# Kernel tuning notes

Hardware: AMD Instinct MI355X
Metric: run time of the kernel (lower is better)

## Reference

```python
import jax, jax.numpy as jnp
import numpy as np

B, N, C_IN = 8, 2048, 64
NUM_TERMS, NUM_CHANNELS = 3, 64
LN_EPS = 1e-5


def setup_inputs() -> dict:
    key = jax.random.key(0)
    k1, k2, k3 = jax.random.split(key, 3)
    A = jax.random.normal(k1, (B, N, N), dtype=jnp.float32) / jnp.sqrt(N).astype(jnp.float32)
    X = jax.random.normal(k2, (B, N, C_IN), dtype=jnp.float32)
    # xavier_uniform on h of shape [num_terms+1, num_channels, num_nodes]
    fan_in, fan_out = NUM_CHANNELS, N
    bound = float(np.sqrt(6.0 / (fan_in + fan_out)))
    h = jax.random.uniform(k3, (NUM_TERMS + 1, NUM_CHANNELS, N), dtype=jnp.float32,
                           minval=-bound, maxval=bound)
    gamma = jnp.ones((NUM_CHANNELS,), dtype=jnp.float32)
    beta = jnp.zeros((NUM_CHANNELS,), dtype=jnp.float32)
    return {"A": A, "X": X, "h": h, "gamma": gamma, "beta": beta}


def reference(A, X, h, gamma, beta):
    # Original loops compute: Y[b,n,c] = sum_i h[i,c,n] * (A^i @ sum_ch X[...,ch])[b,n]
    num_terms = h.shape[0] - 1
    Xs = X.sum(axis=-1)  # [B, N] -- inner channel loop collapses to a sum

    def step(p, _):
        p_next = jnp.einsum('bmn,bn->bm', A, p)  # A^i @ Xs
        return p_next, p_next

    _, Ps = jax.lax.scan(step, Xs, None, length=num_terms)  # [T, B, N]
    P = jnp.concatenate([Xs[None], Ps], axis=0)  # [T+1, B, N], P[0] = I @ Xs

    Y = jnp.einsum('icn,ibn->bnc', h, P)  # [B, N, C]

    mean = Y.mean(axis=-1, keepdims=True)
    var = Y.var(axis=-1, keepdims=True)
    Yn = (Y - mean) * jax.lax.rsqrt(var + LN_EPS) * gamma + beta
    return jnp.tanh(Yn)
```

## Files before the change

kernel.cpp:

```cpp
#include <hip/hip_runtime.h>
#include <hip/hip_bf16.h>
#include <hip/hip_fp16.h>
#include <math.h>

#define BB 8
#define NN 2048
#define C_IN 64
#define NCH 64
#define NTERMS 3
#define LN_EPS 1e-5f

__global__ void xsum_kernel(const float* __restrict__ X, float* __restrict__ Xs) {
    int row  = (blockIdx.x * blockDim.x + threadIdx.x) >> 6;
    int lane = threadIdx.x & 63;
    float v = X[(size_t)row * C_IN + lane];
    #pragma unroll
    for (int off = 32; off > 0; off >>= 1)
        v += __shfl_down(v, off, 64);
    if (lane == 0) Xs[row] = v;
}

__global__ __launch_bounds__(256, 4) void matvec_cvt_kernel(
        const float* __restrict__ A,
        const float* __restrict__ pin,
        float* __restrict__ pout,
        __half* __restrict__ A16) {
    const int b    = blockIdx.y;
    const int wave = threadIdx.x >> 6;
    const int lane = threadIdx.x & 63;
    const int m    = blockIdx.x * 4 + wave;

    const float4* pin4 = (const float4*)(pin + (size_t)b * NN);
    const float4* Ar   = (const float4*)(A + (size_t)b * NN * NN + (size_t)m * NN);

    float4 x[8], pr[8];
    #pragma unroll
    for (int j = 0; j < 8; ++j) x[j]  = Ar[j * 64 + lane];
    #pragma unroll
    for (int j = 0; j < 8; ++j) pr[j] = pin4[j * 64 + lane];

    float acc = 0.f;
    #pragma unroll
    for (int j = 0; j < 8; ++j)
        acc += x[j].x * pr[j].x + x[j].y * pr[j].y + x[j].z * pr[j].z + x[j].w * pr[j].w;

    float2* A16r = (float2*)(A16 + (size_t)b * NN * NN + (size_t)m * NN);
    #pragma unroll
    for (int j = 0; j < 8; ++j) {
        union { float2 f2; __half2 h2[2]; } u;
        u.h2[0] = __floats2half2_rn(x[j].x, x[j].y);
        u.h2[1] = __floats2half2_rn(x[j].z, x[j].w);
        A16r[j * 64 + lane] = u.f2;
    }

    #pragma unroll
    for (int off = 32; off > 0; off >>= 1)
        acc += __shfl_down(acc, off, 64);
    if (lane == 0) pout[(size_t)b * NN + m] = acc;
}

__global__ __launch_bounds__(256, 4) void matvec16_kernel(
        const __half* __restrict__ A16,
        const float* __restrict__ pin,
        float* __restrict__ pout) {
    const int b    = blockIdx.y;
    const int wave = threadIdx.x >> 6;
    const int lane = threadIdx.x & 63;
    const int m    = blockIdx.x * 4 + wave;

    const float4* pin4 = (const float4*)(pin + (size_t)b * NN);
    const float4* Ar   = (const float4*)(A16 + (size_t)b * NN * NN + (size_t)m * NN);

    float4 xr[4], pa[4], pb[4];
    #pragma unroll
    for (int j = 0; j < 4; ++j) xr[j] = Ar[j * 64 + lane];
    #pragma unroll
    for (int j = 0; j < 4; ++j) {
        pa[j] = pin4[2 * (j * 64 + lane)];
        pb[j] = pin4[2 * (j * 64 + lane) + 1];
    }

    float acc = 0.f;
    #pragma unroll
    for (int j = 0; j < 4; ++j) {
        const __half2* hx = (const __half2*)&xr[j];
        float2 f0 = __half22float2(hx[0]);
        float2 f1 = __half22float2(hx[1]);
        float2 f2 = __half22float2(hx[2]);
        float2 f3 = __half22float2(hx[3]);
        acc += f0.x * pa[j].x + f0.y * pa[j].y + f1.x * pa[j].z + f1.y * pa[j].w
             + f2.x * pb[j].x + f2.y * pb[j].y + f3.x * pb[j].z + f3.y * pb[j].w;
    }

    #pragma unroll
    for (int off = 32; off > 0; off >>= 1)
        acc += __shfl_down(acc, off, 64);
    if (lane == 0) pout[(size_t)b * NN + m] = acc;
}

__global__ __launch_bounds__(512) void combine_kernel(
        const float* __restrict__ h,
        const float* __restrict__ P,
        const float* __restrict__ gamma,
        const float* __restrict__ beta,
        float* __restrict__ out) {
    const int n    = blockIdx.x;
    const int b    = threadIdx.x >> 6;
    const int lane = threadIdx.x & 63;
    const int idx  = b * NN + n;

    const float p0 = P[0 * BB * NN + idx];
    const float p1 = P[1 * BB * NN + idx];
    const float p2 = P[2 * BB * NN + idx];
    const float p3 = P[3 * BB * NN + idx];

    float y = h[(size_t)(0 * NCH + lane) * NN + n] * p0
            + h[(size_t)(1 * NCH + lane) * NN + n] * p1
            + h[(size_t)(2 * NCH + lane) * NN + n] * p2
            + h[(size_t)(3 * NCH + lane) * NN + n] * p3;

    float s = y;
    #pragma unroll
    for (int off = 32; off > 0; off >>= 1)
        s += __shfl_xor(s, off, 64);
    const float mean = s * (1.f / NCH);

    float d = y - mean;
    float vs = d * d;
    #pragma unroll
    for (int off = 32; off > 0; off >>= 1)
        vs += __shfl_xor(vs, off, 64);
    const float rstd = rsqrtf(vs * (1.f / NCH) + LN_EPS);

    out[(size_t)idx * NCH + lane] = tanhf(d * rstd * gamma[lane] + beta[lane]);
}

extern "C" void kernel_launch(void* const* d_in, const int* in_sizes, int n_in,
                              void* d_out, int out_size, void* d_ws, size_t ws_size,
                              hipStream_t stream) {
    const float* A     = (const float*)d_in[0];
    const float* X     = (const float*)d_in[1];
    const float* h     = (const float*)d_in[2];
    const float* gamma = (const float*)d_in[3];
    const float* beta  = (const float*)d_in[4];
    float* out = (float*)d_out;

    float*  P   = (float*)d_ws;
    __half* A16 = (__half*)((char*)d_ws + (1u << 20));

    xsum_kernel<<<(BB * NN) / 4, 256, 0, stream>>>(X, P);

    dim3 mv_grid(NN / 4, BB);
    matvec_cvt_kernel<<<mv_grid, 256, 0, stream>>>(A, P, P + BB * NN, A16);

    for (int i = 2; i <= NTERMS; ++i) {
        matvec16_kernel<<<mv_grid, 256, 0, stream>>>(
            A16, P + (size_t)(i - 1) * BB * NN, P + (size_t)i * BB * NN);
    }

    combine_kernel<<<NN, 512, 0, stream>>>(h, P, gamma, beta, out);
}
```

Measured before the change: 249.3 us.

## Fuse all stages into one cooperative persistent kernel with grid syncs

Replaces the five separate launches (channel sum, fp32 matvec with fp16 conversion, two fp16 matvecs, layernorm combine) with one cooperative kernel of 256 blocks of 1024 threads that uses grid.sync between power iterations. Each block stages the input vector in shared memory and keeps its own rows' results in shared memory, so the final combine and layernorm need no extra pass over P. This removes launch gaps and repeated global vector reads, but adds grid-wide barrier cost. Only 256 blocks of 16 waves are used, so each wave processes four rows in sequence, which may cut the memory parallelism available for streaming A.

```diff
diff --git a/kernel.cpp b/kernel.cpp
--- a/kernel.cpp
+++ b/kernel.cpp
@@ -1,138 +1,181 @@
 #include <hip/hip_runtime.h>
-#include <hip/hip_bf16.h>
 #include <hip/hip_fp16.h>
+#include <hip/hip_cooperative_groups.h>
 #include <math.h>
+
+namespace cg = cooperative_groups;
 
 #define BB 8
 #define NN 2048
 #define C_IN 64
 #define NCH 64
-#define NTERMS 3
 #define LN_EPS 1e-5f
 
-__global__ void xsum_kernel(const float* __restrict__ X, float* __restrict__ Xs) {
-    int row  = (blockIdx.x * blockDim.x + threadIdx.x) >> 6;
-    int lane = threadIdx.x & 63;
-    float v = X[(size_t)row * C_IN + lane];
-    #pragma unroll
-    for (int off = 32; off > 0; off >>= 1)
-        v += __shfl_down(v, off, 64);
-    if (lane == 0) Xs[row] = v;
-}
+__global__ __launch_bounds__(1024, 4) void fused_kernel(
+        const float* __restrict__ A,
+        const float* __restrict__ X,
+        const float* __restrict__ h,
+        const float* __restrict__ gamma,
+        const float* __restrict__ beta,
+        float* __restrict__ out,
+        float* __restrict__ P,
+        __half* __restrict__ A16) {
+    cg::grid_group grid = cg::this_grid();
 
-__global__ __launch_bounds__(256, 4) void matvec_cvt_kernel(
-        const float* __restrict__ A,
-        const float* __restrict__ pin,
-        float* __restrict__ pout,
-        __half* __restrict__ A16) {
-    const int b    = blockIdx.y;
+    const int blk  = blockIdx.x;
     const int wave = threadIdx.x >> 6;
     const int lane = threadIdx.x & 63;
-    const int m    = blockIdx.x * 4 + wave;
+    const int b    = blk >> 5;
+    const int n0   = (blk & 31) * 64;
 
-    const float4* pin4 = (const float4*)(pin + (size_t)b * NN);
-    const float4* Ar   = (const float4*)(A + (size_t)b * NN * NN + (size_t)m * NN);
+    __shared__ float p[NN];
+    __shared__ float pl[4][64];
 
-    float4 x[8], pr[8];
     #pragma unroll
-    for (int j = 0; j < 8; ++j) x[j]  = Ar[j * 64 + lane];
-    #pragma unroll
-    for (int j = 0; j < 8; ++j) pr[j] = pin4[j * 64 + lane];
+    for (int i = 0; i < 4; ++i) {
+        const int n = n0 + wave * 4 + i;
+        float v = X[((size_t)b * NN + n) * C_IN + lane];
+        #pragma unroll
+        for (int off = 32; off > 0; off >>= 1)
+            v += __shfl_down(v, off, 64);
+        if (lane == 0) { P[b * NN + n] = v; pl[0][wave * 4 + i] = v; }
+    }
+    grid.sync();
 
-    float acc = 0.f;
-    #pragma unroll
-    for (int j = 0; j < 8; ++j)
-        acc += x[j].x * pr[j].x + x[j].y * pr[j].y + x[j].z * pr[j].z + x[j].w * pr[j].w;
+    {
+        float4* p4 = (float4*)p;
+        const float4* src = (const float4*)(P + b * NN);
+        if (threadIdx.x < NN / 4) p4[threadIdx.x] = src[threadIdx.x];
+        __syncthreads();
 
-    float2* A16r = (float2*)(A16 + (size_t)b * NN * NN + (size_t)m * NN);
-    #pragma unroll
-    for (int j = 0; j < 8; ++j) {
-        union { float2 f2; __half2 h2[2]; } u;
-        u.h2[0] = __floats2half2_rn(x[j].x, x[j].y);
-        u.h2[1] = __floats2half2_rn(x[j].z, x[j].w);
-        A16r[j * 64 + lane] = u.f2;
+        #pragma unroll
+        for (int i = 0; i < 4; ++i) {
+            const int m = n0 + wave * 4 + i;
+            const float4* Ar = (const float4*)(A + (size_t)b * NN * NN + (size_t)m * NN);
+            float4 x[8];
+            #pragma unroll
+            for (int j = 0; j < 8; ++j) x[j] = Ar[j * 64 + lane];
+
+            float acc = 0.f;
+            #pragma unroll
+            for (int j = 0; j < 8; ++j) {
+                float4 pv = p4[j * 64 + lane];
+                acc += x[j].x * pv.x + x[j].y * pv.y + x[j].z * pv.z + x[j].w * pv.w;
+            }
+
+            float2* A16r = (float2*)(A16 + (size_t)b * NN * NN + (size_t)m * NN);
+            #pragma unroll
+            for (int j = 0; j < 8; ++j) {
+                union { float2 f2; __half2 h2[2]; } u;
+                u.h2[0] = __floats2half2_rn(x[j].x, x[j].y);
+                u.h2[1] = __floats2half2_rn(x[j].z, x[j].w);
+                A16r[j * 64 + lane] = u.f2;
+            }
+
+            #pragma unroll
+            for (int off = 32; off > 0; off >>= 1)
+                acc += __shfl_down(acc, off, 64);
+            if (lane == 0) { P[(BB + b) * NN + m] = acc; pl[1][wave * 4 + i] = acc; }
+        }
+    }
+    grid.sync();
+
+    {
+        float4* p4 = (float4*)p;
+        const float4* src = (const float4*)(P + (BB + b) * NN);
+        if (threadIdx.x < NN / 4) p4[threadIdx.x] = src[threadIdx.x];
+        __syncthreads();
+
+        #pragma unroll
+        for (int i = 0; i < 4; ++i) {
+            const int m = n0 + wave * 4 + i;
+            const float4* Ar = (const float4*)(A16 + (size_t)b * NN * NN + (size_t)m * NN);
+            float4 xr[4];
+            #pragma unroll
+            for (int j = 0; j < 4; ++j) xr[j] = Ar[j * 64 + lane];
+
+            float acc = 0.f;
+            #pragma unroll
+            for (int j = 0; j < 4; ++j) {
+                float4 pa = p4[2 * (j * 64 + lane)];
+                float4 pb = p4[2 * (j * 64 + lane) + 1];
+                const __half2* hx = (const __half2*)&xr[j];
+                float2 f0 = __half22float2(hx[0]);
+                float2 f1 = __half22float2(hx[1]);
+                float2 f2 = __half22float2(hx[2]);
+                float2 f3 = __half22float2(hx[3]);
+                acc += f0.x * pa.x + f0.y * pa.y + f1.x * pa.z + f1.y * pa.w
+                     + f2.x * pb.x + f2.y * pb.y + f3.x * pb.z + f3.y * pb.w;
+            }
+
+            #pragma unroll
+            for (int off = 32; off > 0; off >>= 1)
+                acc += __shfl_down(acc, off, 64);
+            if (lane == 0) { P[(2 * BB + b) * NN + m] = acc; pl[2][wave * 4 + i] = acc; }
+        }
+    }
+    grid.sync();
+
+    {
+        float4* p4 = (float4*)p;
+        const float4* src = (const float4*)(P + (2 * BB + b) * NN);
+        if (threadIdx.x < NN / 4) p4[threadIdx.x] = src[threadIdx.x];
+        __syncthreads();
+
+        #pragma unroll
+        for (int i = 0; i < 4; ++i) {
+            const int m = n0 + wave * 4 + i;
+            const float4* Ar = (const float4*)(A16 + (size_t)b * NN * NN + (size_t)m * NN);
+            float4 xr[4];
+            #pragma unroll
+            for (int j = 0; j < 4; ++j) xr[j] = Ar[j * 64 + lane];
+
+            float acc = 0.f;
+            #pragma unroll
+            for (int j = 0; j < 4; ++j) {
+                float4 pa = p4[2 * (j * 64 + lane)];
+                float4 pb = p4[2 * (j * 64 + lane) + 1];
+                const __half2* hx = (const __half2*)&xr[j];
+                float2 f0 = __half22float2(hx[0]);
+                float2 f1 = __half22float2(hx[1]);
+                float2 f2 = __half22float2(hx[2]);
+                float2 f3 = __half22float2(hx[3]);
+                acc += f0.x * pa.x + f0.y * pa.y + f1.x * pa.z + f1.y * pa.w
+                     + f2.x * pb.x + f2.y * pb.y + f3.x * pb.z + f3.y * pb.w;
+            }
+
+            #pragma unroll
+            for (int off = 32; off > 0; off >>= 1)
+                acc += __shfl_down(acc, off, 64);
+            if (lane == 0) pl[3][wave * 4 + i] = acc;
+        }
     }
 
     #pragma unroll
-    for (int off = 32; off > 0; off >>= 1)
-        acc += __shfl_down(acc, off, 64);
-    if (lane == 0) pout[(size_t)b * NN + m] = acc;
-}
+    for (int i = 0; i < 4; ++i) {
+        const int r = wave * 4 + i;
+        const int n = n0 + r;
 
-__global__ __launch_bounds__(256, 4) void matvec16_kernel(
-        const __half* __restrict__ A16,
-        const float* __restrict__ pin,
-        float* __restrict__ pout) {
-    const int b    = blockIdx.y;
-    const int wave = threadIdx.x >> 6;
-    const int lane = threadIdx.x & 63;
-    const int m    = blockIdx.x * 4 + wave;
+        float y = h[(size_t)(0 * NCH + lane) * NN + n] * pl[0][r]
+                + h[(size_t)(1 * NCH + lane) * NN + n] * pl[1][r]
+                + h[(size_t)(2 * NCH + lane) * NN + n] * pl[2][r]
+                + h[(size_t)(3 * NCH + lane) * NN + n] * pl[3][r];
 
-    const float4* pin4 = (const float4*)(pin + (size_t)b * NN);
-    const float4* Ar   = (const float4*)(A16 + (size_t)b * NN * NN + (size_t)m * NN);
+        float s = y;
+        #pragma unroll
+        for (int off = 32; off > 0; off >>= 1)
+            s += __shfl_xor(s, off, 64);
+        const float mean = s * (1.f / NCH);
 
-    float4 xr[4], pa[4], pb[4];
-    #pragma unroll
-    for (int j = 0; j < 4; ++j) xr[j] = Ar[j * 64 + lane];
-    #pragma unroll
-    for (int j = 0; j < 4; ++j) {
-        pa[j] = pin4[2 * (j * 64 + lane)];
-        pb[j] = pin4[2 * (j * 64 + lane) + 1];
+        float d = y - mean;
+        float vs = d * d;
+        #pragma unroll
+        for (int off = 32; off > 0; off >>= 1)
+            vs += __shfl_xor(vs, off, 64);
+        const float rstd = rsqrtf(vs * (1.f / NCH) + LN_EPS);
+
+        out[((size_t)b * NN + n) * NCH + lane] = tanhf(d * rstd * gamma[lane] + beta[lane]);
     }
-
-    float acc = 0.f;
-    #pragma unroll
-    for (int j = 0; j < 4; ++j) {
-        const __half2* hx = (const __half2*)&xr[j];
-        float2 f0 = __half22float2(hx[0]);
-        float2 f1 = __half22float2(hx[1]);
-        float2 f2 = __half22float2(hx[2]);
-        float2 f3 = __half22float2(hx[3]);
-        acc += f0.x * pa[j].x + f0.y * pa[j].y + f1.x * pa[j].z + f1.y * pa[j].w
-             + f2.x * pb[j].x + f2.y * pb[j].y + f3.x * pb[j].z + f3.y * pb[j].w;
-    }
-
-    #pragma unroll
-    for (int off = 32; off > 0; off >>= 1)
-        acc += __shfl_down(acc, off, 64);
-    if (lane == 0) pout[(size_t)b * NN + m] = acc;
-}
-
-__global__ __launch_bounds__(512) void combine_kernel(
-        const float* __restrict__ h,
-        const float* __restrict__ P,
-        const float* __restrict__ gamma,
-        const float* __restrict__ beta,
-        float* __restrict__ out) {
-    const int n    = blockIdx.x;
-    const int b    = threadIdx.x >> 6;
-    const int lane = threadIdx.x & 63;
-    const int idx  = b * NN + n;
-
-    const float p0 = P[0 * BB * NN + idx];
-    const float p1 = P[1 * BB * NN + idx];
-    const float p2 = P[2 * BB * NN + idx];
-    const float p3 = P[3 * BB * NN + idx];
-
-    float y = h[(size_t)(0 * NCH + lane) * NN + n] * p0
-            + h[(size_t)(1 * NCH + lane) * NN + n] * p1
-            + h[(size_t)(2 * NCH + lane) * NN + n] * p2
-            + h[(size_t)(3 * NCH + lane) * NN + n] * p3;
-
-    float s = y;
-    #pragma unroll
-    for (int off = 32; off > 0; off >>= 1)
-        s += __shfl_xor(s, off, 64);
-    const float mean = s * (1.f / NCH);
-
-    float d = y - mean;
-    float vs = d * d;
-    #pragma unroll
-    for (int off = 32; off > 0; off >>= 1)
-        vs += __shfl_xor(vs, off, 64);
-    const float rstd = rsqrtf(vs * (1.f / NCH) + LN_EPS);
-
-    out[(size_t)idx * NCH + lane] = tanhf(d * rstd * gamma[lane] + beta[lane]);
 }
 
 extern "C" void kernel_launch(void* const* d_in, const int* in_sizes, int n_in,
@@ -148,15 +191,8 @@
     float*  P   = (float*)d_ws;
     __half* A16 = (__half*)((char*)d_ws + (1u << 20));
 
-    xsum_kernel<<<(BB * NN) / 4, 256, 0, stream>>>(X, P);
-
-    dim3 mv_grid(NN / 4, BB);
-    matvec_cvt_kernel<<<mv_grid, 256, 0, stream>>>(A, P, P + BB * NN, A16);
-
-    for (int i = 2; i <= NTERMS; ++i) {
-        matvec16_kernel<<<mv_grid, 256, 0, stream>>>(
-            A16, P + (size_t)(i - 1) * BB * NN, P + (size_t)i * BB * NN);
-    }
-
-    combine_kernel<<<NN, 512, 0, stream>>>(h, P, gamma, beta, out);
+    void* args[] = { (void*)&A, (void*)&X, (void*)&h, (void*)&gamma,
+                     (void*)&beta, (void*)&out, (void*)&P, (void*)&A16 };
+    hipLaunchCooperativeKernel((void*)fused_kernel, dim3(256), dim3(1024),
+                               args, 0, stream);
 }
```

After: 347.5 us. 39.4% more time.
